# Performance work log

Measured on AMD Instinct MI355X. Metric: run time of the kernel, lower is better.

Reference implementation:

```python
import jax, jax.numpy as jnp
import numpy as np

HEADS = 8

def _conv1x1(x, W, b):
    # x: [n, Cin, H, W]; W: [Cout, Cin]; b: [Cout]
    return jnp.einsum('nchw,oc->nohw', x, W) + b[None, :, None, None]

def setup_inputs() -> dict:
    key = jax.random.key(0)
    ks = jax.random.split(key, 11)
    n, Cin, H, W = 8, 256, 80, 80
    Ck, Cv = 256, 256
    s_in = 1.0 / np.sqrt(Cin)
    s_v = 1.0 / np.sqrt(Cv)
    return {
        'query_feature': jax.random.normal(ks[0], (n, Cin, H, W), jnp.float32),
        'key_feature': jax.random.normal(ks[1], (n, Cin, H, W), jnp.float32),
        'value_feature': jax.random.normal(ks[2], (n, Cin, H, W), jnp.float32),
        'Wq': jax.random.normal(ks[3], (Ck, Cin), jnp.float32) * s_in,
        'bq': jax.random.normal(ks[4], (Ck,), jnp.float32) * s_in,
        'Wk': jax.random.normal(ks[5], (Ck, Cin), jnp.float32) * s_in,
        'bk': jax.random.normal(ks[6], (Ck,), jnp.float32) * s_in,
        'Wv': jax.random.normal(ks[7], (Cv, Cin), jnp.float32) * s_in,
        'bv': jax.random.normal(ks[8], (Cv,), jnp.float32) * s_in,
        'Wr': jax.random.normal(ks[9], (Cin, Cv), jnp.float32) * s_v,
        'br': jax.random.normal(ks[10], (Cin,), jnp.float32) * s_v,
    }

def reference(query_feature, key_feature, value_feature, Wq, bq, Wk, bk, Wv, bv, Wr, br):
    n, _, qh, qw = query_feature.shape
    kvn, _, kvh, kvw = key_feature.shape
    Ck = Wq.shape[0]
    Cv = Wv.shape[0]
    hk = Ck // HEADS
    hv = Cv // HEADS
    Lq = qh * qw
    Lkv = kvh * kvw
    # 1x1 conv projections, split channels into heads (consecutive channel blocks)
    q = _conv1x1(query_feature, Wq, bq).reshape(n, HEADS, hk, Lq)
    k = _conv1x1(key_feature, Wk, bk).reshape(kvn, HEADS, hk, Lkv)
    v = _conv1x1(value_feature, Wv, bv).reshape(kvn, HEADS, hv, Lkv)
    # softmax: keys over spatial positions, queries over head channels
    k = jax.nn.softmax(k, axis=3)
    q = jax.nn.softmax(q, axis=2)
    # efficient (linear) attention: context = K @ V^T, out = context^T @ Q
    context = jnp.einsum('nhkl,nhvl->nhkv', k, v)          # [n, H, hk, hv]
    attended = jnp.einsum('nhkv,nhkl->nhvl', context, q)   # [n, H, hv, Lq]
    aggregated = attended.reshape(n, Cv, qh, qw)
    return _conv1x1(aggregated, Wr, br) + query_feature
```

## Files before the change

kernel.cpp:

```cpp
#include <hip/hip_runtime.h>
#include <hip/hip_bf16.h>

#define NB 8
#define C 256
#define LL 6400
#define HEADS 8
#define HC 32
#define NH 64
#define CH 40
#define CHUNK 160
#define KCHUNKS 25

typedef unsigned short u16;
typedef unsigned int u32;
typedef __attribute__((ext_vector_type(8))) short bf16x8;
typedef __attribute__((ext_vector_type(4))) float f32x4;

typedef __attribute__((address_space(1))) const u32 ga_u32;
typedef __attribute__((address_space(3))) u32 ls_u32;

__device__ __forceinline__ void gload_lds16(const u16* g, u16* l) {
  __builtin_amdgcn_global_load_lds((ga_u32*)g, (ls_u32*)l, 16, 0, 0);
}

__device__ __forceinline__ float bf2f(u32 u) { return __uint_as_float(u << 16); }
__device__ __forceinline__ u16 f2bf(float f) {
  __hip_bfloat16 h = __float2bfloat16(f);
  return *(u16*)&h;
}
__device__ __forceinline__ void unpack8(uint4 u, float* f) {
  f[0] = bf2f(u.x & 0xffffu); f[1] = bf2f(u.x >> 16);
  f[2] = bf2f(u.y & 0xffffu); f[3] = bf2f(u.y >> 16);
  f[4] = bf2f(u.z & 0xffffu); f[5] = bf2f(u.z >> 16);
  f[6] = bf2f(u.w & 0xffffu); f[7] = bf2f(u.w >> 16);
}

__global__ __launch_bounds__(256) void transpose_cvt(const float* __restrict__ X,
                                                     u16* __restrict__ Xt) {
  __shared__ float tl[64][65];
  const int n = blockIdx.z, l0 = blockIdx.x * 64, c0 = blockIdx.y * 64;
  const int t = threadIdx.x;
  const int rr = t >> 4;
  const int lc = (t & 15) * 4;
  const float* Xn = X + (size_t)n * C * LL;
#pragma unroll
  for (int p = 0; p < 4; ++p) {
    const int row = p * 16 + rr;
    float4 v = *(const float4*)&Xn[(size_t)(c0 + row) * LL + l0 + lc];
    tl[row][lc + 0] = v.x; tl[row][lc + 1] = v.y;
    tl[row][lc + 2] = v.z; tl[row][lc + 3] = v.w;
  }
  __syncthreads();
  u16* XtN = Xt + (size_t)n * LL * C;
  const int cc = (t & 15) * 4;
#pragma unroll
  for (int p = 0; p < 4; ++p) {
    const int lrow = p * 16 + rr;
    ushort4 o;
    o.x = f2bf(tl[cc + 0][lrow]); o.y = f2bf(tl[cc + 1][lrow]);
    o.z = f2bf(tl[cc + 2][lrow]); o.w = f2bf(tl[cc + 3][lrow]);
    *(ushort4*)&XtN[(size_t)(l0 + lrow) * C + c0 + cc] = o;
  }
}

__global__ __launch_bounds__(256) void cvt_bf16(const float* __restrict__ src,
                                                u16* __restrict__ dst) {
  const int i = (blockIdx.x * 256 + threadIdx.x) * 4;
  float4 v = *(const float4*)&src[i];
  ushort4 o = {f2bf(v.x), f2bf(v.y), f2bf(v.z), f2bf(v.w)};
  *(ushort4*)&dst[i] = o;
}

__global__ __launch_bounds__(256) void proj_mfma(const u16* __restrict__ Xt,
    const u16* __restrict__ Wb, const float* __restrict__ bias,
    u16* __restrict__ Pt) {
  __shared__ __align__(16) u16 As[4096];
  __shared__ __align__(16) u16 Bs[4096];
  const int n = blockIdx.z;
  const int l0 = blockIdx.x * 128;
  const int co0 = blockIdx.y * 128;
  const int t = threadIdx.x;
  const int lane = t & 63, wave = t >> 6;
  const int wm = (wave >> 1) * 64, wn = (wave & 1) * 64;
  const int srow = t >> 2;
  const int scol = (t & 3) * 8;
  const u16* XtN = Xt + (size_t)n * LL * C;
  f32x4 acc[4][4] = {};
  for (int k0 = 0; k0 < C; k0 += 32) {
    __syncthreads();
    gload_lds16(&XtN[(size_t)(l0 + srow) * C + k0 + scol], &As[wave * 512]);
    gload_lds16(&XtN[(size_t)(l0 + 64 + srow) * C + k0 + scol], &As[2048 + wave * 512]);
    gload_lds16(&Wb[(size_t)(co0 + srow) * C + k0 + scol], &Bs[wave * 512]);
    gload_lds16(&Wb[(size_t)(co0 + 64 + srow) * C + k0 + scol], &Bs[2048 + wave * 512]);
    __syncthreads();
    const int fr = lane & 15, quad = lane >> 4;
    bf16x8 a[4], b[4];
#pragma unroll
    for (int i = 0; i < 4; ++i)
      a[i] = *(const bf16x8*)&As[(wm + i * 16 + fr) * 32 + quad * 8];
#pragma unroll
    for (int j = 0; j < 4; ++j)
      b[j] = *(const bf16x8*)&Bs[(wn + j * 16 + fr) * 32 + quad * 8];
#pragma unroll
    for (int i = 0; i < 4; ++i)
#pragma unroll
      for (int j = 0; j < 4; ++j)
        acc[i][j] = __builtin_amdgcn_mfma_f32_16x16x32_bf16(a[i], b[j], acc[i][j], 0, 0, 0);
  }
  u16* PtN = Pt + (size_t)n * LL * C;
  const int fr = lane & 15, quad = lane >> 4;
  const int colc = co0 + wn + fr;
  float bv[4];
#pragma unroll
  for (int j = 0; j < 4; ++j) bv[j] = bias[colc + j * 16];
#pragma unroll
  for (int i = 0; i < 4; ++i) {
    const int lrow = l0 + wm + i * 16 + quad * 4;
#pragma unroll
    for (int r = 0; r < 4; ++r)
#pragma unroll
      for (int j = 0; j < 4; ++j)
        PtN[(size_t)(lrow + r) * C + colc + j * 16] = f2bf(acc[i][j][r] + bv[j]);
  }
}

__global__ __launch_bounds__(256) void kstats(const u16* __restrict__ Kt,
    float* __restrict__ pmax, float* __restrict__ psum) {
  const int chk = blockIdx.x, n = blockIdx.y;
  const int t = threadIdx.x;
  const int c2 = t & 127, ph = t >> 7;
  const u16* base = Kt + ((size_t)n * LL + chk * 256) * C + c2 * 2;
  float m0 = -1e30f, m1 = -1e30f;
  for (int i = 0; i < 128; ++i) {
    u32 u = *(const u32*)&base[(size_t)(2 * i + ph) * C];
    m0 = fmaxf(m0, bf2f(u & 0xffffu)); m1 = fmaxf(m1, bf2f(u >> 16));
  }
  __shared__ float sm[2][256];
  sm[ph][c2 * 2] = m0; sm[ph][c2 * 2 + 1] = m1;
  __syncthreads();
  m0 = fmaxf(sm[0][c2 * 2], sm[1][c2 * 2]);
  m1 = fmaxf(sm[0][c2 * 2 + 1], sm[1][c2 * 2 + 1]);
  float s0 = 0.f, s1 = 0.f;
  for (int i = 0; i < 128; ++i) {
    u32 u = *(const u32*)&base[(size_t)(2 * i + ph) * C];
    s0 += __expf(bf2f(u & 0xffffu) - m0);
    s1 += __expf(bf2f(u >> 16) - m1);
  }
  __syncthreads();
  sm[ph][c2 * 2] = s0; sm[ph][c2 * 2 + 1] = s1;
  __syncthreads();
  if (ph == 0) {
    const int idx = (n * KCHUNKS + chk) * 256 + c2 * 2;
    pmax[idx] = m0; pmax[idx + 1] = m1;
    psum[idx] = sm[0][c2 * 2] + sm[1][c2 * 2];
    psum[idx + 1] = sm[0][c2 * 2 + 1] + sm[1][c2 * 2 + 1];
  }
}

__global__ __launch_bounds__(256) void kmerge(const float* __restrict__ pmax,
    const float* __restrict__ psum, float* __restrict__ kmax, float* __restrict__ krs) {
  const int n = blockIdx.x, c = threadIdx.x;
  float m = -1e30f;
  for (int ch = 0; ch < KCHUNKS; ++ch)
    m = fmaxf(m, pmax[(n * KCHUNKS + ch) * 256 + c]);
  float s = 0.f;
  for (int ch = 0; ch < KCHUNKS; ++ch)
    s += psum[(n * KCHUNKS + ch) * 256 + c] * __expf(pmax[(n * KCHUNKS + ch) * 256 + c] - m);
  kmax[n * 256 + c] = m;
  krs[n * 256 + c] = 1.0f / s;
}

__global__ __launch_bounds__(256) void qsoftmax(u16* __restrict__ Qt) {
  const int t = threadIdx.x;
  const int lane = t & 63, wave = t >> 6;
  const int g = lane >> 2, sub = lane & 3;
  const int gid = (blockIdx.x * 4 + wave) * 16 + g;
  const int h = gid & 7;
  const size_t row = (size_t)(gid >> 3);
  u16* p = Qt + row * C + h * 32 + sub * 8;
  uint4 u = *(const uint4*)p;
  float v[8]; unpack8(u, v);
  float m = v[0];
#pragma unroll
  for (int j = 1; j < 8; ++j) m = fmaxf(m, v[j]);
  m = fmaxf(m, __shfl_xor(m, 1));
  m = fmaxf(m, __shfl_xor(m, 2));
  float e[8], s = 0.f;
#pragma unroll
  for (int j = 0; j < 8; ++j) { e[j] = __expf(v[j] - m); s += e[j]; }
  s += __shfl_xor(s, 1);
  s += __shfl_xor(s, 2);
  const float r = 1.0f / s;
  union { uint4 u; u16 h[8]; } o;
#pragma unroll
  for (int j = 0; j < 8; ++j) o.h[j] = f2bf(e[j] * r);
  *(uint4*)p = o.u;
}

__global__ __launch_bounds__(64) void ctx_partial(const u16* __restrict__ Kt,
    const u16* __restrict__ Vt, const float* __restrict__ kmax,
    const float* __restrict__ krs, float* __restrict__ part) {
  __shared__ float Ks[32][36];
  __shared__ float Vs[32][36];
  const int nh = blockIdx.y, chk = blockIdx.x;
  const int n = nh >> 3, h = nh & 7;
  const int lane = threadIdx.x;
  const int rr = lane >> 2, koff = (lane & 3) * 8;
  float km[8];
#pragma unroll
  for (int j = 0; j < 8; ++j) km[j] = kmax[n * C + h * 32 + koff + j];
  const size_t rowbase = ((size_t)n * LL + chk * CHUNK) * C + h * 32 + koff;
  const int k4 = (lane & 7) * 4, v4 = (lane >> 3) * 4;
  float acc[4][4];
#pragma unroll
  for (int i = 0; i < 4; ++i)
#pragma unroll
    for (int j = 0; j < 4; ++j) acc[i][j] = 0.f;
  for (int ls = 0; ls < CHUNK; ls += 32) {
    __syncthreads();
#pragma unroll
    for (int p = 0; p < 2; ++p) {
      const int r = p * 16 + rr;
      uint4 ku = *(const uint4*)&Kt[rowbase + (size_t)(ls + r) * C];
      uint4 vu = *(const uint4*)&Vt[rowbase + (size_t)(ls + r) * C];
      float kf[8], vf[8];
      unpack8(ku, kf); unpack8(vu, vf);
#pragma unroll
      for (int j = 0; j < 8; ++j) {
        Ks[r][koff + j] = __expf(kf[j] - km[j]);
        Vs[r][koff + j] = vf[j];
      }
    }
    __syncthreads();
#pragma unroll
    for (int l = 0; l < 32; ++l) {
      float a[4], b[4];
      *(float4*)a = *(const float4*)&Ks[l][k4];
      *(float4*)b = *(const float4*)&Vs[l][v4];
#pragma unroll
      for (int i = 0; i < 4; ++i)
#pragma unroll
        for (int j = 0; j < 4; ++j) acc[i][j] = fmaf(a[i], b[j], acc[i][j]);
    }
  }
#pragma unroll
  for (int i = 0; i < 4; ++i) {
    const float rs = krs[n * C + h * 32 + k4 + i];
#pragma unroll
    for (int j = 0; j < 4; ++j)
      part[(((size_t)chk * NH + nh) * HC + k4 + i) * HC + v4 + j] = acc[i][j] * rs;
  }
}

__global__ __launch_bounds__(256) void ctx_reduce(const float* __restrict__ part,
                                                  float* __restrict__ ctx) {
  const int idx = blockIdx.x * 256 + threadIdx.x;
  float s = 0.f;
  for (int c = 0; c < CH; ++c) s += part[(size_t)c * (NH * HC * HC) + idx];
  ctx[idx] = s;
}

__global__ __launch_bounds__(256) void mfuse(const float* __restrict__ Wr,
    const float* __restrict__ ctx, u16* __restrict__ M) {
  const int idx = blockIdx.x * 256 + threadIdx.x;
  const int hk = idx & 255;
  const int o = (idx >> 8) & 255;
  const int n = idx >> 16;
  const int h = hk >> 5, k = hk & 31;
  const float* wr = Wr + (size_t)o * C + h * HC;
  const float* cx = ctx + ((size_t)(n * HEADS + h) * HC + k) * HC;
  float s = 0.f;
#pragma unroll
  for (int v = 0; v < HC; ++v) s = fmaf(wr[v], cx[v], s);
  M[idx] = f2bf(s);
}

__global__ __launch_bounds__(256) void out_mfma(const u16* __restrict__ Qt,
    const u16* __restrict__ Mb, const float* __restrict__ br,
    const float* __restrict__ Xq, float* __restrict__ out) {
  __shared__ __align__(16) u16 As[4096];
  __shared__ __align__(16) u16 Bs[4096];
  const int n = blockIdx.z;
  const int l0 = blockIdx.x * 128;
  const int co0 = blockIdx.y * 128;
  const int t = threadIdx.x;
  const int lane = t & 63, wave = t >> 6;
  const int wm = (wave >> 1) * 64, wn = (wave & 1) * 64;
  const int srow = t >> 2;
  const int scol = (t & 3) * 8;
  const u16* MbN = Mb + (size_t)n * C * C;
  const u16* QtN = Qt + (size_t)n * LL * C;
  f32x4 acc[4][4] = {};
  for (int k0 = 0; k0 < C; k0 += 32) {
    __syncthreads();
    gload_lds16(&MbN[(size_t)(co0 + srow) * C + k0 + scol], &As[wave * 512]);
    gload_lds16(&MbN[(size_t)(co0 + 64 + srow) * C + k0 + scol], &As[2048 + wave * 512]);
    gload_lds16(&QtN[(size_t)(l0 + srow) * C + k0 + scol], &Bs[wave * 512]);
    gload_lds16(&QtN[(size_t)(l0 + 64 + srow) * C + k0 + scol], &Bs[2048 + wave * 512]);
    __syncthreads();
    const int fr = lane & 15, quad = lane >> 4;
    bf16x8 a[4], b[4];
#pragma unroll
    for (int i = 0; i < 4; ++i)
      a[i] = *(const bf16x8*)&As[(wm + i * 16 + fr) * 32 + quad * 8];
#pragma unroll
    for (int j = 0; j < 4; ++j)
      b[j] = *(const bf16x8*)&Bs[(wn + j * 16 + fr) * 32 + quad * 8];
#pragma unroll
    for (int i = 0; i < 4; ++i)
#pragma unroll
      for (int j = 0; j < 4; ++j)
        acc[i][j] = __builtin_amdgcn_mfma_f32_16x16x32_bf16(a[i], b[j], acc[i][j], 0, 0, 0);
  }
  const float* XqN = Xq + (size_t)n * C * LL;
  float* On = out + (size_t)n * C * LL;
  const int fr = lane & 15, quad = lane >> 4;
#pragma unroll
  for (int i = 0; i < 4; ++i) {
#pragma unroll
    for (int r = 0; r < 4; ++r) {
      const int co = co0 + wm + i * 16 + quad * 4 + r;
      const float bb = br[co];
#pragma unroll
      for (int j = 0; j < 4; ++j) {
        const int l = l0 + wn + j * 16 + fr;
        const size_t off = (size_t)co * LL + l;
        On[off] = acc[i][j][r] + bb + XqN[off];
      }
    }
  }
}

extern "C" void kernel_launch(void* const* d_in, const int* in_sizes, int n_in,
                              void* d_out, int out_size, void* d_ws, size_t ws_size,
                              hipStream_t stream) {
  const float* Xq = (const float*)d_in[0];
  const float* Xk = (const float*)d_in[1];
  const float* Xv = (const float*)d_in[2];
  const float* Wq = (const float*)d_in[3];
  const float* bq = (const float*)d_in[4];
  const float* Wk = (const float*)d_in[5];
  const float* bk = (const float*)d_in[6];
  const float* Wv = (const float*)d_in[7];
  const float* bv = (const float*)d_in[8];
  const float* Wr = (const float*)d_in[9];
  const float* br = (const float*)d_in[10];
  float* out = (float*)d_out;

  char* ws = (char*)d_ws;
  const size_t nelem = (size_t)NB * LL * C;
  u16* Xt = (u16*)ws;
  u16* Qt = (u16*)(ws + nelem * 2);
  u16* Kt = (u16*)(ws + nelem * 4);
  u16* Vt = (u16*)(ws + nelem * 6);
  char* p = ws + nelem * 8;
  u16* Wqb = (u16*)p; p += C * C * 2;
  u16* Wkb = (u16*)p; p += C * C * 2;
  u16* Wvb = (u16*)p; p += C * C * 2;
  u16* Mb = (u16*)p;  p += (size_t)NB * C * C * 2;
  float* pmax = (float*)p; p += KCHUNKS * NB * C * 4;
  float* psum = (float*)p; p += KCHUNKS * NB * C * 4;
  float* kmax = (float*)p; p += NB * C * 4;
  float* krs = (float*)p;  p += NB * C * 4;
  float* ctx = (float*)p;  p += NH * HC * HC * 4;
  float* part = (float*)p;

  const dim3 gT(100, 4, NB);
  const dim3 gG(50, 2, NB);

  cvt_bf16<<<64, 256, 0, stream>>>(Wq, Wqb);
  cvt_bf16<<<64, 256, 0, stream>>>(Wk, Wkb);
  cvt_bf16<<<64, 256, 0, stream>>>(Wv, Wvb);

  transpose_cvt<<<gT, 256, 0, stream>>>(Xq, Xt);
  proj_mfma<<<gG, 256, 0, stream>>>(Xt, Wqb, bq, Qt);
  transpose_cvt<<<gT, 256, 0, stream>>>(Xk, Xt);
  proj_mfma<<<gG, 256, 0, stream>>>(Xt, Wkb, bk, Kt);
  transpose_cvt<<<gT, 256, 0, stream>>>(Xv, Xt);
  proj_mfma<<<gG, 256, 0, stream>>>(Xt, Wvb, bv, Vt);

  qsoftmax<<<NB * LL * HEADS / 64, 256, 0, stream>>>(Qt);
  kstats<<<dim3(KCHUNKS, NB), 256, 0, stream>>>(Kt, pmax, psum);
  kmerge<<<NB, 256, 0, stream>>>(pmax, psum, kmax, krs);
  ctx_partial<<<dim3(CH, NH), 64, 0, stream>>>(Kt, Vt, kmax, krs, part);
  ctx_reduce<<<NH * HC * HC / 256, 256, 0, stream>>>(part, ctx);
  mfuse<<<NB * C * C / 256, 256, 0, stream>>>(Wr, ctx, Mb);
  out_mfma<<<gG, 256, 0, stream>>>(Qt, Mb, br, Xq, out);
}
```

Before: 359.1 us.

## Batch Q/K/V projections, fuse softmaxes and context reductions, cut kernel launches

Merges the three transpose and three projection launches into single batched launches over q/k/v, and converts the fp32 weights to bf16 inline while staging them into LDS. The Q softmax moves into the output GEMM's operand load, the K-stat merge and the context reduction move into a fused context kernel with 4 segments per head, and mfuse sums those 4 partials. This removes many small launches and a full read-modify-write pass over Q. In exchange, the context kernel runs only 256 blocks, the Q softmax is recomputed once per output-channel tile (twice per element), and the workspace grows to hold three separate transposed inputs.

```diff
diff --git a/kernel.cpp b/kernel.cpp
--- a/kernel.cpp
+++ b/kernel.cpp
@@ -7,8 +7,6 @@
 #define HEADS 8
 #define HC 32
 #define NH 64
-#define CH 40
-#define CHUNK 160
 #define KCHUNKS 25
 
 typedef unsigned short u16;
@@ -35,14 +33,17 @@
   f[6] = bf2f(u.w & 0xffffu); f[7] = bf2f(u.w >> 16);
 }
 
-__global__ __launch_bounds__(256) void transpose_cvt(const float* __restrict__ X,
-                                                     u16* __restrict__ Xt) {
+struct TransArgs { const float* X[3]; u16* Xt[3]; };
+struct ProjArgs { const u16* Xt[3]; const float* W[3]; const float* bias[3]; u16* P[3]; };
+
+__global__ __launch_bounds__(256) void trans3(TransArgs args) {
   __shared__ float tl[64][65];
-  const int n = blockIdx.z, l0 = blockIdx.x * 64, c0 = blockIdx.y * 64;
+  const int which = blockIdx.z >> 3, n = blockIdx.z & 7;
+  const int l0 = blockIdx.x * 64, c0 = blockIdx.y * 64;
   const int t = threadIdx.x;
   const int rr = t >> 4;
   const int lc = (t & 15) * 4;
-  const float* Xn = X + (size_t)n * C * LL;
+  const float* Xn = args.X[which] + (size_t)n * C * LL;
 #pragma unroll
   for (int p = 0; p < 4; ++p) {
     const int row = p * 16 + rr;
@@ -51,7 +52,7 @@
     tl[row][lc + 2] = v.z; tl[row][lc + 3] = v.w;
   }
   __syncthreads();
-  u16* XtN = Xt + (size_t)n * LL * C;
+  u16* XtN = args.Xt[which] + (size_t)n * LL * C;
   const int cc = (t & 15) * 4;
 #pragma unroll
   for (int p = 0; p < 4; ++p) {
@@ -63,35 +64,40 @@
   }
 }
 
-__global__ __launch_bounds__(256) void cvt_bf16(const float* __restrict__ src,
-                                                u16* __restrict__ dst) {
-  const int i = (blockIdx.x * 256 + threadIdx.x) * 4;
-  float4 v = *(const float4*)&src[i];
-  ushort4 o = {f2bf(v.x), f2bf(v.y), f2bf(v.z), f2bf(v.w)};
-  *(ushort4*)&dst[i] = o;
-}
-
-__global__ __launch_bounds__(256) void proj_mfma(const u16* __restrict__ Xt,
-    const u16* __restrict__ Wb, const float* __restrict__ bias,
-    u16* __restrict__ Pt) {
+__global__ __launch_bounds__(256) void proj3(ProjArgs args) {
   __shared__ __align__(16) u16 As[4096];
   __shared__ __align__(16) u16 Bs[4096];
-  const int n = blockIdx.z;
-  const int l0 = blockIdx.x * 128;
-  const int co0 = blockIdx.y * 128;
+  const int which = blockIdx.z >> 3, n = blockIdx.z & 7;
+  const int co0 = blockIdx.x * 128;
+  const int l0 = blockIdx.y * 128;
   const int t = threadIdx.x;
   const int lane = t & 63, wave = t >> 6;
   const int wm = (wave >> 1) * 64, wn = (wave & 1) * 64;
   const int srow = t >> 2;
   const int scol = (t & 3) * 8;
-  const u16* XtN = Xt + (size_t)n * LL * C;
+  const int brow = t >> 1;
+  const int bkh = (t & 1) * 16;
+  const u16* XtN = args.Xt[which] + (size_t)n * LL * C;
+  const float* W = args.W[which];
   f32x4 acc[4][4] = {};
   for (int k0 = 0; k0 < C; k0 += 32) {
     __syncthreads();
     gload_lds16(&XtN[(size_t)(l0 + srow) * C + k0 + scol], &As[wave * 512]);
     gload_lds16(&XtN[(size_t)(l0 + 64 + srow) * C + k0 + scol], &As[2048 + wave * 512]);
-    gload_lds16(&Wb[(size_t)(co0 + srow) * C + k0 + scol], &Bs[wave * 512]);
-    gload_lds16(&Wb[(size_t)(co0 + 64 + srow) * C + k0 + scol], &Bs[2048 + wave * 512]);
+    {
+      const float* wp = &W[(size_t)(co0 + brow) * C + k0 + bkh];
+      float4 w0 = *(const float4*)&wp[0];
+      float4 w1 = *(const float4*)&wp[4];
+      float4 w2 = *(const float4*)&wp[8];
+      float4 w3 = *(const float4*)&wp[12];
+      union { uint4 u; u16 h[8]; } p0, p1;
+      p0.h[0] = f2bf(w0.x); p0.h[1] = f2bf(w0.y); p0.h[2] = f2bf(w0.z); p0.h[3] = f2bf(w0.w);
+      p0.h[4] = f2bf(w1.x); p0.h[5] = f2bf(w1.y); p0.h[6] = f2bf(w1.z); p0.h[7] = f2bf(w1.w);
+      p1.h[0] = f2bf(w2.x); p1.h[1] = f2bf(w2.y); p1.h[2] = f2bf(w2.z); p1.h[3] = f2bf(w2.w);
+      p1.h[4] = f2bf(w3.x); p1.h[5] = f2bf(w3.y); p1.h[6] = f2bf(w3.z); p1.h[7] = f2bf(w3.w);
+      *(uint4*)&Bs[brow * 32 + bkh] = p0.u;
+      *(uint4*)&Bs[brow * 32 + bkh + 8] = p1.u;
+    }
     __syncthreads();
     const int fr = lane & 15, quad = lane >> 4;
     bf16x8 a[4], b[4];
@@ -107,7 +113,8 @@
       for (int j = 0; j < 4; ++j)
         acc[i][j] = __builtin_amdgcn_mfma_f32_16x16x32_bf16(a[i], b[j], acc[i][j], 0, 0, 0);
   }
-  u16* PtN = Pt + (size_t)n * LL * C;
+  u16* PtN = args.P[which] + (size_t)n * LL * C;
+  const float* bias = args.bias[which];
   const int fr = lane & 15, quad = lane >> 4;
   const int colc = co0 + wn + fr;
   float bv[4];
@@ -157,86 +164,56 @@
   }
 }
 
-__global__ __launch_bounds__(256) void kmerge(const float* __restrict__ pmax,
-    const float* __restrict__ psum, float* __restrict__ kmax, float* __restrict__ krs) {
-  const int n = blockIdx.x, c = threadIdx.x;
-  float m = -1e30f;
-  for (int ch = 0; ch < KCHUNKS; ++ch)
-    m = fmaxf(m, pmax[(n * KCHUNKS + ch) * 256 + c]);
-  float s = 0.f;
-  for (int ch = 0; ch < KCHUNKS; ++ch)
-    s += psum[(n * KCHUNKS + ch) * 256 + c] * __expf(pmax[(n * KCHUNKS + ch) * 256 + c] - m);
-  kmax[n * 256 + c] = m;
-  krs[n * 256 + c] = 1.0f / s;
-}
-
-__global__ __launch_bounds__(256) void qsoftmax(u16* __restrict__ Qt) {
-  const int t = threadIdx.x;
-  const int lane = t & 63, wave = t >> 6;
-  const int g = lane >> 2, sub = lane & 3;
-  const int gid = (blockIdx.x * 4 + wave) * 16 + g;
-  const int h = gid & 7;
-  const size_t row = (size_t)(gid >> 3);
-  u16* p = Qt + row * C + h * 32 + sub * 8;
-  uint4 u = *(const uint4*)p;
-  float v[8]; unpack8(u, v);
-  float m = v[0];
-#pragma unroll
-  for (int j = 1; j < 8; ++j) m = fmaxf(m, v[j]);
-  m = fmaxf(m, __shfl_xor(m, 1));
-  m = fmaxf(m, __shfl_xor(m, 2));
-  float e[8], s = 0.f;
-#pragma unroll
-  for (int j = 0; j < 8; ++j) { e[j] = __expf(v[j] - m); s += e[j]; }
-  s += __shfl_xor(s, 1);
-  s += __shfl_xor(s, 2);
-  const float r = 1.0f / s;
-  union { uint4 u; u16 h[8]; } o;
-#pragma unroll
-  for (int j = 0; j < 8; ++j) o.h[j] = f2bf(e[j] * r);
-  *(uint4*)p = o.u;
-}
-
-__global__ __launch_bounds__(64) void ctx_partial(const u16* __restrict__ Kt,
-    const u16* __restrict__ Vt, const float* __restrict__ kmax,
-    const float* __restrict__ krs, float* __restrict__ part) {
-  __shared__ float Ks[32][36];
-  __shared__ float Vs[32][36];
-  const int nh = blockIdx.y, chk = blockIdx.x;
+__global__ __launch_bounds__(256) void ctx_fused(const u16* __restrict__ Kt,
+    const u16* __restrict__ Vt, const float* __restrict__ pmax,
+    const float* __restrict__ psum, float* __restrict__ part) {
+  __shared__ float kms[HC], krss[HC];
+  __shared__ float Ks[4][16][36];
+  __shared__ float Vs[4][16][36];
+  __shared__ float red[4][HC][HC];
+  const int nh = blockIdx.y, seg = blockIdx.x;
   const int n = nh >> 3, h = nh & 7;
-  const int lane = threadIdx.x;
-  const int rr = lane >> 2, koff = (lane & 3) * 8;
+  const int t = threadIdx.x, w = t >> 6, lane = t & 63;
+  if (t < HC) {
+    const int c = h * HC + t;
+    float m = -1e30f;
+    for (int ch = 0; ch < KCHUNKS; ++ch)
+      m = fmaxf(m, pmax[(n * KCHUNKS + ch) * C + c]);
+    float s = 0.f;
+    for (int ch = 0; ch < KCHUNKS; ++ch)
+      s += psum[(n * KCHUNKS + ch) * C + c] * __expf(pmax[(n * KCHUNKS + ch) * C + c] - m);
+    kms[t] = m; krss[t] = 1.0f / s;
+  }
+  __syncthreads();
+  const int r16 = lane >> 2, coff = (lane & 3) * 8;
   float km[8];
 #pragma unroll
-  for (int j = 0; j < 8; ++j) km[j] = kmax[n * C + h * 32 + koff + j];
-  const size_t rowbase = ((size_t)n * LL + chk * CHUNK) * C + h * 32 + koff;
+  for (int j = 0; j < 8; ++j) km[j] = kms[coff + j];
   const int k4 = (lane & 7) * 4, v4 = (lane >> 3) * 4;
   float acc[4][4];
 #pragma unroll
   for (int i = 0; i < 4; ++i)
 #pragma unroll
     for (int j = 0; j < 4; ++j) acc[i][j] = 0.f;
-  for (int ls = 0; ls < CHUNK; ls += 32) {
-    __syncthreads();
-#pragma unroll
-    for (int p = 0; p < 2; ++p) {
-      const int r = p * 16 + rr;
-      uint4 ku = *(const uint4*)&Kt[rowbase + (size_t)(ls + r) * C];
-      uint4 vu = *(const uint4*)&Vt[rowbase + (size_t)(ls + r) * C];
-      float kf[8], vf[8];
-      unpack8(ku, kf); unpack8(vu, vf);
-#pragma unroll
-      for (int j = 0; j < 8; ++j) {
-        Ks[r][koff + j] = __expf(kf[j] - km[j]);
-        Vs[r][koff + j] = vf[j];
-      }
-    }
-    __syncthreads();
-#pragma unroll
-    for (int l = 0; l < 32; ++l) {
+  for (int it = 0; it < 25; ++it) {
+    const int lbase = seg * 1600 + (it * 4 + w) * 16;
+    const size_t off = ((size_t)n * LL + lbase + r16) * C + h * HC + coff;
+    uint4 ku = *(const uint4*)&Kt[off];
+    uint4 vu = *(const uint4*)&Vt[off];
+    float kf[8], vf[8];
+    unpack8(ku, kf); unpack8(vu, vf);
+    __syncthreads();
+#pragma unroll
+    for (int j = 0; j < 8; ++j) {
+      Ks[w][r16][coff + j] = __expf(kf[j] - km[j]);
+      Vs[w][r16][coff + j] = vf[j];
+    }
+    __syncthreads();
+#pragma unroll
+    for (int l = 0; l < 16; ++l) {
       float a[4], b[4];
-      *(float4*)a = *(const float4*)&Ks[l][k4];
-      *(float4*)b = *(const float4*)&Vs[l][v4];
+      *(float4*)a = *(const float4*)&Ks[w][l][k4];
+      *(float4*)b = *(const float4*)&Vs[w][l][v4];
 #pragma unroll
       for (int i = 0; i < 4; ++i)
 #pragma unroll
@@ -245,49 +222,55 @@
   }
 #pragma unroll
   for (int i = 0; i < 4; ++i) {
-    const float rs = krs[n * C + h * 32 + k4 + i];
-#pragma unroll
-    for (int j = 0; j < 4; ++j)
-      part[(((size_t)chk * NH + nh) * HC + k4 + i) * HC + v4 + j] = acc[i][j] * rs;
-  }
-}
-
-__global__ __launch_bounds__(256) void ctx_reduce(const float* __restrict__ part,
-                                                  float* __restrict__ ctx) {
-  const int idx = blockIdx.x * 256 + threadIdx.x;
-  float s = 0.f;
-  for (int c = 0; c < CH; ++c) s += part[(size_t)c * (NH * HC * HC) + idx];
-  ctx[idx] = s;
+    const float rs = krss[k4 + i];
+#pragma unroll
+    for (int j = 0; j < 4; ++j) red[w][k4 + i][v4 + j] = acc[i][j] * rs;
+  }
+  __syncthreads();
+  const float* rf = &red[0][0][0];
+  const int e0 = t * 4;
+  float4 o;
+  o.x = rf[e0 + 0] + rf[1024 + e0 + 0] + rf[2048 + e0 + 0] + rf[3072 + e0 + 0];
+  o.y = rf[e0 + 1] + rf[1024 + e0 + 1] + rf[2048 + e0 + 1] + rf[3072 + e0 + 1];
+  o.z = rf[e0 + 2] + rf[1024 + e0 + 2] + rf[2048 + e0 + 2] + rf[3072 + e0 + 2];
+  o.w = rf[e0 + 3] + rf[1024 + e0 + 3] + rf[2048 + e0 + 3] + rf[3072 + e0 + 3];
+  *(float4*)&part[((size_t)seg * NH + nh) * (HC * HC) + e0] = o;
 }
 
 __global__ __launch_bounds__(256) void mfuse(const float* __restrict__ Wr,
-    const float* __restrict__ ctx, u16* __restrict__ M) {
+    const float* __restrict__ part, u16* __restrict__ M) {
   const int idx = blockIdx.x * 256 + threadIdx.x;
   const int hk = idx & 255;
   const int o = (idx >> 8) & 255;
   const int n = idx >> 16;
   const int h = hk >> 5, k = hk & 31;
   const float* wr = Wr + (size_t)o * C + h * HC;
-  const float* cx = ctx + ((size_t)(n * HEADS + h) * HC + k) * HC;
+  const float* p0 = part + ((size_t)(n * HEADS + h)) * (HC * HC) + k * HC;
+  const size_t segstr = (size_t)NH * HC * HC;
   float s = 0.f;
 #pragma unroll
-  for (int v = 0; v < HC; ++v) s = fmaf(wr[v], cx[v], s);
+  for (int v = 0; v < HC; ++v) {
+    float cv = p0[v] + p0[segstr + v] + p0[2 * segstr + v] + p0[3 * segstr + v];
+    s = fmaf(wr[v], cv, s);
+  }
   M[idx] = f2bf(s);
 }
 
-__global__ __launch_bounds__(256) void out_mfma(const u16* __restrict__ Qt,
+__global__ __launch_bounds__(256) void out3(const u16* __restrict__ Qt,
     const u16* __restrict__ Mb, const float* __restrict__ br,
     const float* __restrict__ Xq, float* __restrict__ out) {
   __shared__ __align__(16) u16 As[4096];
   __shared__ __align__(16) u16 Bs[4096];
   const int n = blockIdx.z;
-  const int l0 = blockIdx.x * 128;
-  const int co0 = blockIdx.y * 128;
+  const int co0 = blockIdx.x * 128;
+  const int l0 = blockIdx.y * 128;
   const int t = threadIdx.x;
   const int lane = t & 63, wave = t >> 6;
   const int wm = (wave >> 1) * 64, wn = (wave & 1) * 64;
   const int srow = t >> 2;
   const int scol = (t & 3) * 8;
+  const int brow = t >> 2;
+  const int bsc = (t & 3) * 8;
   const u16* MbN = Mb + (size_t)n * C * C;
   const u16* QtN = Qt + (size_t)n * LL * C;
   f32x4 acc[4][4] = {};
@@ -295,8 +278,27 @@
     __syncthreads();
     gload_lds16(&MbN[(size_t)(co0 + srow) * C + k0 + scol], &As[wave * 512]);
     gload_lds16(&MbN[(size_t)(co0 + 64 + srow) * C + k0 + scol], &As[2048 + wave * 512]);
-    gload_lds16(&QtN[(size_t)(l0 + srow) * C + k0 + scol], &Bs[wave * 512]);
-    gload_lds16(&QtN[(size_t)(l0 + 64 + srow) * C + k0 + scol], &Bs[2048 + wave * 512]);
+#pragma unroll
+    for (int p = 0; p < 2; ++p) {
+      const int row = p * 64 + brow;
+      uint4 u = *(const uint4*)&QtN[(size_t)(l0 + row) * C + k0 + bsc];
+      float v[8]; unpack8(u, v);
+      float m = v[0];
+#pragma unroll
+      for (int j = 1; j < 8; ++j) m = fmaxf(m, v[j]);
+      m = fmaxf(m, __shfl_xor(m, 1));
+      m = fmaxf(m, __shfl_xor(m, 2));
+      float e[8], s = 0.f;
+#pragma unroll
+      for (int j = 0; j < 8; ++j) { e[j] = __expf(v[j] - m); s += e[j]; }
+      s += __shfl_xor(s, 1);
+      s += __shfl_xor(s, 2);
+      const float r = 1.0f / s;
+      union { uint4 u; u16 h[8]; } o;
+#pragma unroll
+      for (int j = 0; j < 8; ++j) o.h[j] = f2bf(e[j] * r);
+      *(uint4*)&Bs[row * 32 + bsc] = o.u;
+    }
     __syncthreads();
     const int fr = lane & 15, quad = lane >> 4;
     bf16x8 a[4], b[4];
@@ -349,41 +351,32 @@
 
   char* ws = (char*)d_ws;
   const size_t nelem = (size_t)NB * LL * C;
-  u16* Xt = (u16*)ws;
-  u16* Qt = (u16*)(ws + nelem * 2);
-  u16* Kt = (u16*)(ws + nelem * 4);
-  u16* Vt = (u16*)(ws + nelem * 6);
-  char* p = ws + nelem * 8;
-  u16* Wqb = (u16*)p; p += C * C * 2;
-  u16* Wkb = (u16*)p; p += C * C * 2;
-  u16* Wvb = (u16*)p; p += C * C * 2;
-  u16* Mb = (u16*)p;  p += (size_t)NB * C * C * 2;
+  u16* Xtq = (u16*)ws;
+  u16* Xtk = (u16*)(ws + nelem * 2);
+  u16* Xtv = (u16*)(ws + nelem * 4);
+  u16* Qt = (u16*)(ws + nelem * 6);
+  u16* Kt = (u16*)(ws + nelem * 8);
+  u16* Vt = (u16*)(ws + nelem * 10);
+  char* p = ws + nelem * 12;
   float* pmax = (float*)p; p += KCHUNKS * NB * C * 4;
   float* psum = (float*)p; p += KCHUNKS * NB * C * 4;
-  float* kmax = (float*)p; p += NB * C * 4;
-  float* krs = (float*)p;  p += NB * C * 4;
-  float* ctx = (float*)p;  p += NH * HC * HC * 4;
-  float* part = (float*)p;
-
-  const dim3 gT(100, 4, NB);
-  const dim3 gG(50, 2, NB);
-
-  cvt_bf16<<<64, 256, 0, stream>>>(Wq, Wqb);
-  cvt_bf16<<<64, 256, 0, stream>>>(Wk, Wkb);
-  cvt_bf16<<<64, 256, 0, stream>>>(Wv, Wvb);
-
-  transpose_cvt<<<gT, 256, 0, stream>>>(Xq, Xt);
-  proj_mfma<<<gG, 256, 0, stream>>>(Xt, Wqb, bq, Qt);
-  transpose_cvt<<<gT, 256, 0, stream>>>(Xk, Xt);
-  proj_mfma<<<gG, 256, 0, stream>>>(Xt, Wkb, bk, Kt);
-  transpose_cvt<<<gT, 256, 0, stream>>>(Xv, Xt);
-  proj_mfma<<<gG, 256, 0, stream>>>(Xt, Wvb, bv, Vt);
-
-  qsoftmax<<<NB * LL * HEADS / 64, 256, 0, stream>>>(Qt);
+  float* part = (float*)p; p += (size_t)4 * NH * HC * HC * 4;
+  u16* Mb = (u16*)p;
+
+  TransArgs ta;
+  ta.X[0] = Xq; ta.X[1] = Xk; ta.X[2] = Xv;
+  ta.Xt[0] = Xtq; ta.Xt[1] = Xtk; ta.Xt[2] = Xtv;
+  trans3<<<dim3(100, 4, 24), 256, 0, stream>>>(ta);
+
+  ProjArgs pa;
+  pa.Xt[0] = Xtq; pa.Xt[1] = Xtk; pa.Xt[2] = Xtv;
+  pa.W[0] = Wq; pa.W[1] = Wk; pa.W[2] = Wv;
+  pa.bias[0] = bq; pa.bias[1] = bk; pa.bias[2] = bv;
+  pa.P[0] = Qt; pa.P[1] = Kt; pa.P[2] = Vt;
+  proj3<<<dim3(2, 50, 24), 256, 0, stream>>>(pa);
+
   kstats<<<dim3(KCHUNKS, NB), 256, 0, stream>>>(Kt, pmax, psum);
-  kmerge<<<NB, 256, 0, stream>>>(pmax, psum, kmax, krs);
-  ctx_partial<<<dim3(CH, NH), 64, 0, stream>>>(Kt, Vt, kmax, krs, part);
-  ctx_reduce<<<NH * HC * HC / 256, 256, 0, stream>>>(part, ctx);
-  mfuse<<<NB * C * C / 256, 256, 0, stream>>>(Wr, ctx, Mb);
-  out_mfma<<<gG, 256, 0, stream>>>(Qt, Mb, br, Xq, out);
-}
+  ctx_fused<<<dim3(4, NH), 256, 0, stream>>>(Kt, Vt, pmax, psum, part);
+  mfuse<<<NB * C * C / 256, 256, 0, stream>>>(Wr, part, Mb);
+  out3<<<dim3(2, 50, NB), 256, 0, stream>>>(Qt, Mb, br, Xq, out);
+}
```

Result: slower. 405.4 us (+12.9%).
